# Kernel tuning notes

Hardware: AMD Instinct MI355X
Metric: run time of the kernel (lower is better)

Reference implementation:

```python
import jax, jax.numpy as jnp
import numpy as np

B = 256        # number of trees
L0 = 4096      # leaves per tree
L1 = 256       # layer-1 nodes per tree
D = 128        # input_dim == hidden_dim
OUT = 32       # output classes
EPS = 1e-5
N0 = B * L0    # 1,048,576 total leaves
N1 = B * L1    # 65,536 layer-1 nodes
N2 = B         # one root per tree


def _bn(x, g, b):
    # training-mode BatchNorm1d: biased variance over the node axis
    m = jnp.mean(x, axis=0)
    v = jnp.mean((x - m) ** 2, axis=0)
    return g * (x - m) * jax.lax.rsqrt(v + EPS) + b


def _mlp(h, w1, b1, g, beta, w2, b2):
    # GIN-style 2-layer MLP: relu(bn(linear)) -> linear
    return jax.nn.relu(_bn(h @ w1 + b1, g, beta)) @ w2 + b2


def setup_inputs() -> dict:
    key = jax.random.key(0)
    ks = jax.random.split(key, 16)

    def lin(k, fin, fout):
        kw, kb = jax.random.split(k)
        s = 1.0 / np.sqrt(fin)
        return (jax.random.uniform(kw, (fin, fout), jnp.float32, -s, s),
                jax.random.uniform(kb, (fout,), jnp.float32, -s, s))

    x = jax.random.normal(ks[0], (N0, D), jnp.float32)
    # structured tree indices: contiguous children per parent, contiguous trees
    parent1 = jnp.arange(N0, dtype=jnp.int64) // (L0 // L1)   # leaf -> layer1 parent (global)
    parent2 = jnp.arange(N1, dtype=jnp.int64) // L1           # layer1 -> root (global)
    tree0 = jnp.arange(N0, dtype=jnp.int64) // L0             # leaf -> tree id
    tree1 = jnp.arange(N1, dtype=jnp.int64) // L1             # layer1 node -> tree id

    m1w1, m1b1 = lin(ks[1], D, D)
    m1w2, m1b2 = lin(ks[2], D, D)
    m2w1, m2b1 = lin(ks[3], D, D)
    m2w2, m2b2 = lin(ks[4], D, D)
    wp, bp = lin(ks[5], D + 2 * D, OUT)

    ones = jnp.ones((D,), jnp.float32)
    zeros = jnp.zeros((D,), jnp.float32)
    return {
        "x": x, "parent1": parent1, "parent2": parent2, "tree0": tree0, "tree1": tree1,
        "mlp1_w1": m1w1, "mlp1_b1": m1b1, "mlp1_g": ones, "mlp1_beta": zeros,
        "mlp1_w2": m1w2, "mlp1_b2": m1b2, "bn1_g": ones, "bn1_b": zeros,
        "mlp2_w1": m2w1, "mlp2_b1": m2b1, "mlp2_g": ones, "mlp2_beta": zeros,
        "mlp2_w2": m2w2, "mlp2_b2": m2b2, "bn2_g": ones, "bn2_b": zeros,
        "wp": wp, "bp": bp,
    }


def reference(x, parent1, parent2, tree0, tree1,
              mlp1_w1, mlp1_b1, mlp1_g, mlp1_beta, mlp1_w2, mlp1_b2, bn1_g, bn1_b,
              mlp2_w1, mlp2_b1, mlp2_g, mlp2_beta, mlp2_w2, mlp2_b2, bn2_g, bn2_b,
              wp, bp):
    # layer 1: sparse child-sum (spmm with all-ones tree adjacency == segment_sum)
    p1 = jax.ops.segment_sum(x, parent1, num_segments=N1)              # [N1, D]
    h1 = jax.nn.relu(_bn(_mlp(p1, mlp1_w1, mlp1_b1, mlp1_g, mlp1_beta, mlp1_w2, mlp1_b2), bn1_g, bn1_b))
    # layer 2 (roots)
    p2 = jax.ops.segment_sum(h1, parent2, num_segments=N2)             # [B, D]
    h2 = jax.nn.relu(_bn(_mlp(p2, mlp2_w1, mlp2_b1, mlp2_g, mlp2_beta, mlp2_w2, mlp2_b2), bn2_g, bn2_b))
    # tree sum-pooling of layers 0..depth-1; layer depth is already per-tree
    g0 = jax.ops.segment_sum(x, tree0, num_segments=B)                 # [B, D]
    g1 = jax.ops.segment_sum(h1, tree1, num_segments=B)                # [B, D]
    rep = jnp.concatenate([g0, g1, h2], axis=1)                        # [B, 3D]
    return jax.nn.softmax(rep @ wp + bp, axis=1)                       # [B, OUT]
```

## Files before the change

kernel.cpp:

```cpp
#include <hip/hip_runtime.h>
#include <math.h>

#define D      128
#define D4     32
#define NTREE  256
#define NL1    65536
#define EPSBN  1e-5f

#define SC_OFF 0L
#define SD_OFF 256L
#define G0_OFF 512L
#define P2_OFF 33280L
#define ZERO_CNT 66048
#define SA_OFF 66048L
#define SB_OFF 66304L
#define T2_OFF 66560L
#define PBA_OFF 99328L
#define PBB_OFF 361472L
#define WT1_OFF 623616L
#define WT2_OFF 631808L
#define T1_OFF  640000L
#define U_OFF   4834304L

#define FMA4(A_, S_, W_) { (A_).x = fmaf((S_),(W_).x,(A_).x); (A_).y = fmaf((S_),(W_).y,(A_).y); \
                           (A_).z = fmaf((S_),(W_).z,(A_).z); (A_).w = fmaf((S_),(W_).w,(A_).w); }
#define ADD4(A_, B_)     { (A_).x += (B_).x; (A_).y += (B_).y; (A_).z += (B_).z; (A_).w += (B_).w; }
#define F4Z              make_float4(0.f,0.f,0.f,0.f)

typedef short  bf16x8 __attribute__((ext_vector_type(8)));
typedef float  f32x4  __attribute__((ext_vector_type(4)));

__device__ __forceinline__ unsigned short f2b(float f) {
    unsigned u = __float_as_uint(f);
    return (unsigned short)((u + 0x7FFFu + ((u >> 16) & 1u)) >> 16);
}
__device__ __forceinline__ float b2f(unsigned short h) {
    return __uint_as_float(((unsigned)h) << 16);
}

__global__ __launch_bounds__(256) void k_zp(float* __restrict__ ws,
        const float* __restrict__ w1, const float* __restrict__ w2,
        unsigned short* __restrict__ wT1, unsigned short* __restrict__ wT2)
{
    const int b = blockIdx.x, t = threadIdx.x;
    if (b < 258) {
        int i = b * 256 + t;
        if (i < ZERO_CNT) ws[i] = 0.f;
    } else {
        int idx = (b - 258) * 256 + t;
        int mat = idx >> 14;
        int e   = idx & 16383;
        int n = e >> 7, k = e & 127;
        const float* wsrc = mat ? w2 : w1;
        unsigned short* wd = mat ? wT2 : wT1;
        wd[n*128 + k] = f2b(wsrc[k*128 + n]);
    }
}

__global__ __launch_bounds__(256, 6) void k_fused1(const float* __restrict__ x,
        const unsigned short* __restrict__ wT1, const float* __restrict__ b1,
        unsigned short* __restrict__ t1, float* __restrict__ g0,
        float* __restrict__ pbufA)
{
    __shared__ __align__(16) unsigned short tileu[64][136];
    __shared__ __align__(16) float g0red[4][D];
    const int t = threadIdx.x, b = blockIdx.x;
    const int w  = t >> 6;
    const int ln = t & 63;
    const int lc = ln & 31;
    const float4* __restrict__ x4 = (const float4*)x;

    float4 gacc = F4Z;
    #pragma unroll
    for (int pp = 0; pp < 4; ++pp) {
        const int p0 = pp * 16 + w * 4;
        #pragma unroll
        for (int r = 0; r < 4; ++r) {
            const long prow = (long)b * 64 + p0 + r;
            const long base = prow * 512 + ln;
            float4 a = F4Z;
            #pragma unroll
            for (int j = 0; j < 8; ++j) { float4 v = x4[base + j * 64]; ADD4(a, v) }
            float4 o;
            o.x = __shfl_xor(a.x, 32); o.y = __shfl_xor(a.y, 32);
            o.z = __shfl_xor(a.z, 32); o.w = __shfl_xor(a.w, 32);
            ADD4(a, o)
            if (ln < 32) {
                ushort4 h;
                h.x = f2b(a.x); h.y = f2b(a.y); h.z = f2b(a.z); h.w = f2b(a.w);
                *(ushort4*)&tileu[p0 + r][lc*4] = h;
                ADD4(gacc, a)
            }
        }
    }
    if (ln < 32) *(float4*)&g0red[w][lc*4] = gacc;
    __syncthreads();
    if (t < 32) {
        float4 G = F4Z;
        #pragma unroll
        for (int g = 0; g < 4; ++g) { float4 vg = *(const float4*)&g0red[g][t*4]; ADD4(G, vg) }
        const int tree = b >> 2;
        atomicAdd(&g0[tree*D + t*4+0], G.x); atomicAdd(&g0[tree*D + t*4+1], G.y);
        atomicAdd(&g0[tree*D + t*4+2], G.z); atomicAdd(&g0[tree*D + t*4+3], G.w);
    }

    const int lq = ln >> 4;
    const int lr = ln & 15;
    bf16x8 av[4];
    #pragma unroll
    for (int ks = 0; ks < 4; ++ks)
        av[ks] = *(const bf16x8*)&tileu[w*16 + lr][ks*32 + lq*8];
    __syncthreads();

    const long rowbase = (long)b * 64;
    float sP[8], qP[8];
    #pragma unroll
    for (int cb = 0; cb < 8; ++cb) {
        f32x4 acc = {0.f, 0.f, 0.f, 0.f};
        #pragma unroll
        for (int ks = 0; ks < 4; ++ks) {
            bf16x8 bv = *(const bf16x8*)&wT1[(cb*16 + lr)*128 + ks*32 + lq*8];
            acc = __builtin_amdgcn_mfma_f32_16x16x32_bf16(av[ks], bv, acc, 0, 0, 0);
        }
        const float bc = b1[cb*16 + lr];
        float s = 0.f, q = 0.f;
        #pragma unroll
        for (int j = 0; j < 4; ++j) {
            float v = acc[j] + bc;
            t1[(rowbase + w*16 + lq*4 + j)*128 + cb*16 + lr] = f2b(v);
            s += v; q = fmaf(v, v, q);
        }
        sP[cb] = s; qP[cb] = q;
    }

    float* sq = (float*)tileu;
    #pragma unroll
    for (int cb = 0; cb < 8; ++cb) {
        sq[(w*4 + lq)*128 + cb*16 + lr]        = sP[cb];
        sq[2048 + (w*4 + lq)*128 + cb*16 + lr] = qP[cb];
    }
    __syncthreads();
    if (t < 128) {
        float S = 0.f, Q = 0.f;
        #pragma unroll
        for (int r = 0; r < 16; ++r) { S += sq[r*128 + t]; Q += sq[2048 + r*128 + t]; }
        pbufA[b*256 + t]       = S;
        pbufA[b*256 + 128 + t] = Q;
    }
}

__global__ __launch_bounds__(256) void k_statR(const float* __restrict__ pbuf,
                                               float* __restrict__ stats)
{
    __shared__ float red[8][32];
    const int t = threadIdx.x, b = blockIdx.x;
    const int c = b * 32 + (t & 31);
    const int g = t >> 5;
    float s = 0.f;
    #pragma unroll 8
    for (int r = g; r < 1024; r += 8) s += pbuf[r*256 + c];
    red[g][t & 31] = s;
    __syncthreads();
    if (t < 32) {
        float S = 0.f;
        #pragma unroll
        for (int gg = 0; gg < 8; ++gg) S += red[gg][t];
        stats[b*32 + t] = S;
    }
}

__global__ __launch_bounds__(256, 6) void k_mm2(const unsigned short* __restrict__ t1,
        const unsigned short* __restrict__ wT2, const float* __restrict__ b2,
        const float* __restrict__ mg, const float* __restrict__ mbe,
        const float* __restrict__ statsA, unsigned short* __restrict__ u,
        float* __restrict__ pbufB)
{
    __shared__ __align__(16) unsigned short tileu[64][136];
    const int t = threadIdx.x, b = blockIdx.x;
    const int tc = t & 31, rg = t >> 5;
    const long base = (long)b * 64;

    float4 scv, shv;
    {
        const float inv = 1.f / (float)NL1;
        #pragma unroll
        for (int i = 0; i < 4; ++i) {
            const int c = tc*4 + i;
            float m  = statsA[c] * inv;
            float vv = statsA[D + c] * inv - m * m;
            float rs = rsqrtf(vv + EPSBN);
            float sc = mg[c] * rs;
            ((float*)&scv)[i] = sc;
            ((float*)&shv)[i] = mbe[c] - m * sc;
        }
    }
    #pragma unroll
    for (int i = 0; i < 8; ++i) {
        const int row = i * 8 + rg;
        ushort4 hv = *(const ushort4*)&t1[(base + row)*128 + tc*4];
        float4 y;
        y.x = fmaxf(fmaf(b2f(hv.x), scv.x, shv.x), 0.f);
        y.y = fmaxf(fmaf(b2f(hv.y), scv.y, shv.y), 0.f);
        y.z = fmaxf(fmaf(b2f(hv.z), scv.z, shv.z), 0.f);
        y.w = fmaxf(fmaf(b2f(hv.w), scv.w, shv.w), 0.f);
        ushort4 h;
        h.x = f2b(y.x); h.y = f2b(y.y); h.z = f2b(y.z); h.w = f2b(y.w);
        *(ushort4*)&tileu[row][tc*4] = h;
    }
    __syncthreads();

    const int w  = t >> 6;
    const int ln = t & 63;
    const int lq = ln >> 4, lr = ln & 15;
    bf16x8 av[4];
    #pragma unroll
    for (int ks = 0; ks < 4; ++ks)
        av[ks] = *(const bf16x8*)&tileu[w*16 + lr][ks*32 + lq*8];
    __syncthreads();

    float sP[8], qP[8];
    #pragma unroll
    for (int cb = 0; cb < 8; ++cb) {
        f32x4 acc = {0.f, 0.f, 0.f, 0.f};
        #pragma unroll
        for (int ks = 0; ks < 4; ++ks) {
            bf16x8 bv = *(const bf16x8*)&wT2[(cb*16 + lr)*128 + ks*32 + lq*8];
            acc = __builtin_amdgcn_mfma_f32_16x16x32_bf16(av[ks], bv, acc, 0, 0, 0);
        }
        const float bc = b2[cb*16 + lr];
        float s = 0.f, q = 0.f;
        #pragma unroll
        for (int j = 0; j < 4; ++j) {
            float v = acc[j] + bc;
            u[(base + w*16 + lq*4 + j)*128 + cb*16 + lr] = f2b(v);
            s += v; q = fmaf(v, v, q);
        }
        sP[cb] = s; qP[cb] = q;
    }

    float* sq = (float*)tileu;
    #pragma unroll
    for (int cb = 0; cb < 8; ++cb) {
        sq[(w*4 + lq)*128 + cb*16 + lr]        = sP[cb];
        sq[2048 + (w*4 + lq)*128 + cb*16 + lr] = qP[cb];
    }
    __syncthreads();
    if (t < 128) {
        float S = 0.f, Q = 0.f;
        #pragma unroll
        for (int r = 0; r < 16; ++r) { S += sq[r*128 + t]; Q += sq[2048 + r*128 + t]; }
        pbufB[b*256 + t]       = S;
        pbufB[b*256 + 128 + t] = Q;
    }
}

__global__ __launch_bounds__(256) void k_pool(const unsigned short* __restrict__ u,
        const float* __restrict__ bg, const float* __restrict__ bb_,
        const float* __restrict__ statsB, float* __restrict__ p2)
{
    __shared__ __align__(16) float red[8][D];
    const int t = threadIdx.x, b = blockIdx.x;
    const int tree = b >> 3, chunk = b & 7;
    const int tc = t & 31, rr = t >> 5;
    const ushort4* __restrict__ uv = (const ushort4*)u;

    float4 scv, shv;
    {
        const float inv = 1.f / (float)NL1;
        #pragma unroll
        for (int i = 0; i < 4; ++i) {
            const int c = tc*4 + i;
            float m  = statsB[c] * inv;
            float vv = statsB[D + c] * inv - m * m;
            float rs = rsqrtf(vv + EPSBN);
            float sc = bg[c] * rs;
            ((float*)&scv)[i] = sc;
            ((float*)&shv)[i] = bb_[c] - m * sc;
        }
    }
    const long rbase = (long)tree * 256 + chunk * 32;
    float4 ps = F4Z;
    #pragma unroll
    for (int i = 0; i < 4; ++i) {
        const int row = i * 8 + rr;
        ushort4 hv = uv[(rbase + row) * D4 + tc];
        float4 v = make_float4(b2f(hv.x), b2f(hv.y), b2f(hv.z), b2f(hv.w));
        ps.x += fmaxf(fmaf(v.x, scv.x, shv.x), 0.f);
        ps.y += fmaxf(fmaf(v.y, scv.y, shv.y), 0.f);
        ps.z += fmaxf(fmaf(v.z, scv.z, shv.z), 0.f);
        ps.w += fmaxf(fmaf(v.w, scv.w, shv.w), 0.f);
    }
    *(float4*)&red[rr][tc*4] = ps;
    __syncthreads();
    if (t < 32) {
        float4 S = F4Z;
        #pragma unroll
        for (int g = 0; g < 8; ++g) { float4 vs = *(const float4*)&red[g][t*4]; ADD4(S, vs) }
        atomicAdd(&p2[tree*D + t*4+0], S.x); atomicAdd(&p2[tree*D + t*4+1], S.y);
        atomicAdd(&p2[tree*D + t*4+2], S.z); atomicAdd(&p2[tree*D + t*4+3], S.w);
    }
}

__global__ __launch_bounds__(256) void k_root1(const float* __restrict__ p2,
        const float* __restrict__ w1, const float* __restrict__ b1,
        float* __restrict__ t2, float* __restrict__ statsC)
{
    __shared__ __align__(16) float ps[8][D];
    __shared__ __align__(16) float red[2][8][D];
    const int t = threadIdx.x, b = blockIdx.x;
    const int j4 = t & 31, rr = t >> 5;
    *(float4*)&ps[rr][j4*4] = ((const float4*)p2)[(b*8 + rr)*D4 + j4];
    __syncthreads();
    const int row = t >> 5, tc = t & 31;
    const float4* wv = (const float4*)w1;
    float4 acc = ((const float4*)b1)[tc];
    #pragma unroll 8
    for (int k4 = 0; k4 < 32; ++k4) {
        float4 a = *(const float4*)&ps[row][k4*4];
        float4 wr0 = wv[(k4*4+0)*D4 + tc];
        float4 wr1 = wv[(k4*4+1)*D4 + tc];
        float4 wr2 = wv[(k4*4+2)*D4 + tc];
        float4 wr3 = wv[(k4*4+3)*D4 + tc];
        FMA4(acc, a.x, wr0) FMA4(acc, a.y, wr1) FMA4(acc, a.z, wr2) FMA4(acc, a.w, wr3)
    }
    ((float4*)t2)[(b*8 + row)*D4 + tc] = acc;
    float4 q;
    q.x = acc.x*acc.x; q.y = acc.y*acc.y; q.z = acc.z*acc.z; q.w = acc.w*acc.w;
    *(float4*)&red[0][row][tc*4] = acc;
    *(float4*)&red[1][row][tc*4] = q;
    __syncthreads();
    if (t < D) {
        float S = 0.f, Q = 0.f;
        #pragma unroll
        for (int g = 0; g < 8; ++g) { S += red[0][g][t]; Q += red[1][g][t]; }
        atomicAdd(&statsC[t], S);
        atomicAdd(&statsC[D+t], Q);
    }
}

__global__ __launch_bounds__(256) void k_root2(float* __restrict__ t2,
        const float* __restrict__ mg, const float* __restrict__ mb,
        const float* __restrict__ statsC,
        const float* __restrict__ w2, const float* __restrict__ b2,
        float* __restrict__ statsD)
{
    __shared__ __align__(16) float ysr[8][D];
    __shared__ __align__(16) float red[2][8][D];
    __shared__ __align__(16) float scs[D], shs[D];
    const int t = threadIdx.x, b = blockIdx.x;
    if (t < D) {
        float m = statsC[t] * (1.f / 256.f);
        float v = statsC[D+t] * (1.f / 256.f) - m * m;
        float rs = rsqrtf(v + EPSBN);
        float sc = mg[t] * rs;
        scs[t] = sc;
        shs[t] = mb[t] - m * sc;
    }
    __syncthreads();
    const int j4 = t & 31, rr = t >> 5;
    {
        float4 uu = ((const float4*)t2)[(b*8 + rr)*D4 + j4];
        float4 sc4 = *(const float4*)&scs[j4*4];
        float4 sh4 = *(const float4*)&shs[j4*4];
        float4 y;
        y.x = fmaxf(fmaf(uu.x, sc4.x, sh4.x), 0.f);
        y.y = fmaxf(fmaf(uu.y, sc4.y, sh4.y), 0.f);
        y.z = fmaxf(fmaf(uu.z, sc4.z, sh4.z), 0.f);
        y.w = fmaxf(fmaf(uu.w, sc4.w, sh4.w), 0.f);
        *(float4*)&ysr[rr][j4*4] = y;
    }
    __syncthreads();
    const int row = t >> 5, tc = t & 31;
    const float4* wv = (const float4*)w2;
    float4 acc = ((const float4*)b2)[tc];
    #pragma unroll 8
    for (int k4 = 0; k4 < 32; ++k4) {
        float4 a = *(const float4*)&ysr[row][k4*4];
        float4 wr0 = wv[(k4*4+0)*D4 + tc];
        float4 wr1 = wv[(k4*4+1)*D4 + tc];
        float4 wr2 = wv[(k4*4+2)*D4 + tc];
        float4 wr3 = wv[(k4*4+3)*D4 + tc];
        FMA4(acc, a.x, wr0) FMA4(acc, a.y, wr1) FMA4(acc, a.z, wr2) FMA4(acc, a.w, wr3)
    }
    ((float4*)t2)[(b*8 + row)*D4 + tc] = acc;
    float4 q;
    q.x = acc.x*acc.x; q.y = acc.y*acc.y; q.z = acc.z*acc.z; q.w = acc.w*acc.w;
    *(float4*)&red[0][row][tc*4] = acc;
    *(float4*)&red[1][row][tc*4] = q;
    __syncthreads();
    if (t < D) {
        float S = 0.f, Q = 0.f;
        #pragma unroll
        for (int g = 0; g < 8; ++g) { S += red[0][g][t]; Q += red[1][g][t]; }
        atomicAdd(&statsD[t], S);
        atomicAdd(&statsD[D+t], Q);
    }
}

__global__ __launch_bounds__(128) void k_final(const float* __restrict__ u2,
        const float* __restrict__ statsD,
        const float* __restrict__ bg, const float* __restrict__ bb_,
        const float* __restrict__ g0, const float* __restrict__ p2,
        const float* __restrict__ wp, const float* __restrict__ bp,
        float* __restrict__ out)
{
    __shared__ __align__(16) float reps[3*D];
    const int t = threadIdx.x, tree = blockIdx.x;
    if (t < D) {
        float m = statsD[t] * (1.f / 256.f);
        float v = statsD[D+t] * (1.f / 256.f) - m * m;
        float rs = rsqrtf(v + EPSBN);
        float sc = bg[t] * rs;
        float sh = bb_[t] - m * sc;
        reps[2*D + t] = fmaxf(fmaf(u2[tree*D + t], sc, sh), 0.f);
        reps[t]       = g0[tree*D + t];
        reps[D + t]   = p2[tree*D + t];
    }
    __syncthreads();
    if (t < 32) {
        float acc = bp[t];
        #pragma unroll 8
        for (int j = 0; j < 3*D; ++j) acc = fmaf(reps[j], wp[j*32 + t], acc);
        float mx = acc;
        #pragma unroll
        for (int mk = 16; mk > 0; mk >>= 1) mx = fmaxf(mx, __shfl_xor(mx, mk));
        float e = expf(acc - mx);
        float s = e;
        #pragma unroll
        for (int mk = 16; mk > 0; mk >>= 1) s += __shfl_xor(s, mk);
        out[tree*32 + t] = e / s;
    }
}

extern "C" void kernel_launch(void* const* d_in, const int* in_sizes, int n_in,
                              void* d_out, int out_size, void* d_ws, size_t ws_size,
                              hipStream_t stream)
{
    const float* x    = (const float*)d_in[0];
    const float* m1w1 = (const float*)d_in[5];
    const float* m1b1 = (const float*)d_in[6];
    const float* m1g  = (const float*)d_in[7];
    const float* m1be = (const float*)d_in[8];
    const float* m1w2 = (const float*)d_in[9];
    const float* m1b2 = (const float*)d_in[10];
    const float* bn1g = (const float*)d_in[11];
    const float* bn1b = (const float*)d_in[12];
    const float* m2w1 = (const float*)d_in[13];
    const float* m2b1 = (const float*)d_in[14];
    const float* m2g  = (const float*)d_in[15];
    const float* m2be = (const float*)d_in[16];
    const float* m2w2 = (const float*)d_in[17];
    const float* m2b2 = (const float*)d_in[18];
    const float* bn2g = (const float*)d_in[19];
    const float* bn2b = (const float*)d_in[20];
    const float* wp   = (const float*)d_in[21];
    const float* bp   = (const float*)d_in[22];
    float* out = (float*)d_out;
    float* ws  = (float*)d_ws;

    float* sC  = ws + SC_OFF;
    float* sD  = ws + SD_OFF;
    float* g0  = ws + G0_OFF;
    float* p2  = ws + P2_OFF;
    float* sA  = ws + SA_OFF;
    float* sB  = ws + SB_OFF;
    float* t2  = ws + T2_OFF;
    float* pbA = ws + PBA_OFF;
    float* pbB = ws + PBB_OFF;
    unsigned short* wT1 = (unsigned short*)(ws + WT1_OFF);
    unsigned short* wT2 = (unsigned short*)(ws + WT2_OFF);
    unsigned short* t1  = (unsigned short*)(ws + T1_OFF);
    unsigned short* u   = (unsigned short*)(ws + U_OFF);

    hipLaunchKernelGGL(k_zp,     dim3(386),  dim3(256), 0, stream, ws, m1w1, m1w2, wT1, wT2);
    hipLaunchKernelGGL(k_fused1, dim3(1024), dim3(256), 0, stream, x, wT1, m1b1, t1, g0, pbA);
    hipLaunchKernelGGL(k_statR,  dim3(8),    dim3(256), 0, stream, pbA, sA);
    hipLaunchKernelGGL(k_mm2,    dim3(1024), dim3(256), 0, stream, t1, wT2, m1b2, m1g, m1be, sA, u, pbB);
    hipLaunchKernelGGL(k_statR,  dim3(8),    dim3(256), 0, stream, pbB, sB);
    hipLaunchKernelGGL(k_pool,   dim3(2048), dim3(256), 0, stream, u, bn1g, bn1b, sB, p2);
    hipLaunchKernelGGL(k_root1,  dim3(32),   dim3(256), 0, stream, p2, m2w1, m2b1, t2, sC);
    hipLaunchKernelGGL(k_root2,  dim3(32),   dim3(256), 0, stream, t2, m2g, m2be, sC, m2w2, m2b2, sD);
    hipLaunchKernelGGL(k_final,  dim3(256),  dim3(128), 0, stream, t2, sD, bn2g, bn2b, g0, p2, wp, bp, out);
}
```

Measured before the change: 210.9 us.

## Fold stat reductions into producers and merge root kernels via cooperative launch

The separate column-reduction kernels for the BN statistics are removed. Each producer kernel now bumps an atomic counter, and the last block to finish sums the per-block partials into the stats. The three small root/final kernels are merged into one cooperative kernel that uses grid-wide syncs, with a fallback to separate launches if the cooperative launch fails. This is meant to cut launch overhead and dependency gaps between tiny kernels. The cost is that the last-block reduction runs serially in one block, and the grid barriers add their own cost.

```diff
diff --git a/kernel.cpp b/kernel.cpp
--- a/kernel.cpp
+++ b/kernel.cpp
@@ -1,5 +1,8 @@
 #include <hip/hip_runtime.h>
+#include <hip/hip_cooperative_groups.h>
 #include <math.h>
+
+namespace cg = cooperative_groups;
 
 #define D      128
 #define D4     32
@@ -7,20 +10,21 @@
 #define NL1    65536
 #define EPSBN  1e-5f
 
-#define SC_OFF 0L
-#define SD_OFF 256L
-#define G0_OFF 512L
-#define P2_OFF 33280L
-#define ZERO_CNT 66048
-#define SA_OFF 66048L
-#define SB_OFF 66304L
-#define T2_OFF 66560L
-#define PBA_OFF 99328L
-#define PBB_OFF 361472L
-#define WT1_OFF 623616L
-#define WT2_OFF 631808L
-#define T1_OFF  640000L
-#define U_OFF   4834304L
+#define SC_OFF  0L
+#define SD_OFF  256L
+#define G0_OFF  512L
+#define P2_OFF  33280L
+#define CNT_OFF 66048L
+#define ZERO_CNT 66056
+#define SA_OFF  66304L
+#define SB_OFF  66560L
+#define T2_OFF  66816L
+#define PBA_OFF 99584L
+#define PBB_OFF 361728L
+#define WT1_OFF 623872L
+#define WT2_OFF 632064L
+#define T1_OFF  640256L
+#define U_OFF   4834560L
 
 #define FMA4(A_, S_, W_) { (A_).x = fmaf((S_),(W_).x,(A_).x); (A_).y = fmaf((S_),(W_).y,(A_).y); \
                            (A_).z = fmaf((S_),(W_).z,(A_).z); (A_).w = fmaf((S_),(W_).w,(A_).w); }
@@ -43,11 +47,11 @@
         unsigned short* __restrict__ wT1, unsigned short* __restrict__ wT2)
 {
     const int b = blockIdx.x, t = threadIdx.x;
-    if (b < 258) {
+    if (b < 259) {
         int i = b * 256 + t;
         if (i < ZERO_CNT) ws[i] = 0.f;
     } else {
-        int idx = (b - 258) * 256 + t;
+        int idx = (b - 259) * 256 + t;
         int mat = idx >> 14;
         int e   = idx & 16383;
         int n = e >> 7, k = e & 127;
@@ -60,10 +64,12 @@
 __global__ __launch_bounds__(256, 6) void k_fused1(const float* __restrict__ x,
         const unsigned short* __restrict__ wT1, const float* __restrict__ b1,
         unsigned short* __restrict__ t1, float* __restrict__ g0,
-        float* __restrict__ pbufA)
+        float* __restrict__ pbufA, int* __restrict__ cnt,
+        float* __restrict__ statsA)
 {
     __shared__ __align__(16) unsigned short tileu[64][136];
     __shared__ __align__(16) float g0red[4][D];
+    __shared__ bool amLast;
     const int t = threadIdx.x, b = blockIdx.x;
     const int w  = t >> 6;
     const int ln = t & 63;
@@ -104,8 +110,7 @@
         atomicAdd(&g0[tree*D + t*4+2], G.z); atomicAdd(&g0[tree*D + t*4+3], G.w);
     }
 
-    const int lq = ln >> 4;
-    const int lr = ln & 15;
+    const int lq = ln >> 4, lr = ln & 15;
     bf16x8 av[4];
     #pragma unroll
     for (int ks = 0; ks < 4; ++ks)
@@ -147,25 +152,16 @@
         pbufA[b*256 + t]       = S;
         pbufA[b*256 + 128 + t] = Q;
     }
-}
-
-__global__ __launch_bounds__(256) void k_statR(const float* __restrict__ pbuf,
-                                               float* __restrict__ stats)
-{
-    __shared__ float red[8][32];
-    const int t = threadIdx.x, b = blockIdx.x;
-    const int c = b * 32 + (t & 31);
-    const int g = t >> 5;
-    float s = 0.f;
-    #pragma unroll 8
-    for (int r = g; r < 1024; r += 8) s += pbuf[r*256 + c];
-    red[g][t & 31] = s;
-    __syncthreads();
-    if (t < 32) {
+
+    __threadfence();
+    if (t == 0) amLast = (atomicAdd(cnt, 1) == 1023);
+    __syncthreads();
+    if (amLast) {
+        __threadfence();
         float S = 0.f;
-        #pragma unroll
-        for (int gg = 0; gg < 8; ++gg) S += red[gg][t];
-        stats[b*32 + t] = S;
+        #pragma unroll 8
+        for (int r = 0; r < 1024; ++r) S += pbufA[r*256 + t];
+        statsA[t] = S;
     }
 }
 
@@ -173,9 +169,11 @@
         const unsigned short* __restrict__ wT2, const float* __restrict__ b2,
         const float* __restrict__ mg, const float* __restrict__ mbe,
         const float* __restrict__ statsA, unsigned short* __restrict__ u,
-        float* __restrict__ pbufB)
+        float* __restrict__ pbufB, int* __restrict__ cnt,
+        float* __restrict__ statsB)
 {
     __shared__ __align__(16) unsigned short tileu[64][136];
+    __shared__ bool amLast;
     const int t = threadIdx.x, b = blockIdx.x;
     const int tc = t & 31, rg = t >> 5;
     const long base = (long)b * 64;
@@ -252,6 +250,17 @@
         pbufB[b*256 + t]       = S;
         pbufB[b*256 + 128 + t] = Q;
     }
+
+    __threadfence();
+    if (t == 0) amLast = (atomicAdd(cnt, 1) == 1023);
+    __syncthreads();
+    if (amLast) {
+        __threadfence();
+        float S = 0.f;
+        #pragma unroll 8
+        for (int r = 0; r < 1024; ++r) S += pbufB[r*256 + t];
+        statsB[t] = S;
+    }
 }
 
 __global__ __launch_bounds__(256) void k_pool(const unsigned short* __restrict__ u,
@@ -301,13 +310,11 @@
     }
 }
 
-__global__ __launch_bounds__(256) void k_root1(const float* __restrict__ p2,
+__device__ __forceinline__ void root1_body(const float* __restrict__ p2,
         const float* __restrict__ w1, const float* __restrict__ b1,
-        float* __restrict__ t2, float* __restrict__ statsC)
-{
-    __shared__ __align__(16) float ps[8][D];
-    __shared__ __align__(16) float red[2][8][D];
-    const int t = threadIdx.x, b = blockIdx.x;
+        float* __restrict__ t2, float* __restrict__ statsC,
+        float (*ps)[D], float (*red)[8][D], int t, int b)
+{
     const int j4 = t & 31, rr = t >> 5;
     *(float4*)&ps[rr][j4*4] = ((const float4*)p2)[(b*8 + rr)*D4 + j4];
     __syncthreads();
@@ -338,16 +345,13 @@
     }
 }
 
-__global__ __launch_bounds__(256) void k_root2(float* __restrict__ t2,
+__device__ __forceinline__ void root2_body(float* __restrict__ t2,
         const float* __restrict__ mg, const float* __restrict__ mb,
         const float* __restrict__ statsC,
         const float* __restrict__ w2, const float* __restrict__ b2,
-        float* __restrict__ statsD)
-{
-    __shared__ __align__(16) float ysr[8][D];
-    __shared__ __align__(16) float red[2][8][D];
-    __shared__ __align__(16) float scs[D], shs[D];
-    const int t = threadIdx.x, b = blockIdx.x;
+        float* __restrict__ statsD,
+        float (*ysr)[D], float (*red)[8][D], float* scs, float* shs, int t, int b)
+{
     if (t < D) {
         float m = statsC[t] * (1.f / 256.f);
         float v = statsC[D+t] * (1.f / 256.f) - m * m;
@@ -397,15 +401,13 @@
     }
 }
 
-__global__ __launch_bounds__(128) void k_final(const float* __restrict__ u2,
+__device__ __forceinline__ void final_body(const float* __restrict__ u2,
         const float* __restrict__ statsD,
         const float* __restrict__ bg, const float* __restrict__ bb_,
         const float* __restrict__ g0, const float* __restrict__ p2,
         const float* __restrict__ wp, const float* __restrict__ bp,
-        float* __restrict__ out)
-{
-    __shared__ __align__(16) float reps[3*D];
-    const int t = threadIdx.x, tree = blockIdx.x;
+        float* __restrict__ out, float* reps, int t, int tree)
+{
     if (t < D) {
         float m = statsD[t] * (1.f / 256.f);
         float v = statsD[D+t] * (1.f / 256.f) - m * m;
@@ -430,6 +432,64 @@
         for (int mk = 16; mk > 0; mk >>= 1) s += __shfl_xor(s, mk);
         out[tree*32 + t] = e / s;
     }
+}
+
+__global__ __launch_bounds__(256) void k_rootfin(const float* __restrict__ p2,
+        const float* __restrict__ w1, const float* __restrict__ b1,
+        const float* __restrict__ mg, const float* __restrict__ mbe,
+        const float* __restrict__ w2, const float* __restrict__ b2,
+        const float* __restrict__ bg, const float* __restrict__ bb_,
+        const float* __restrict__ g0, const float* __restrict__ wp,
+        const float* __restrict__ bp,
+        float* __restrict__ t2, float* __restrict__ statsC,
+        float* __restrict__ statsD, float* __restrict__ out)
+{
+    cg::grid_group grid = cg::this_grid();
+    __shared__ __align__(16) float ps[8][D];
+    __shared__ __align__(16) float red[2][8][D];
+    __shared__ __align__(16) float scs[D], shs[D];
+    __shared__ __align__(16) float reps[3*D];
+    const int t = threadIdx.x, b = blockIdx.x;
+
+    if (b < 32) root1_body(p2, w1, b1, t2, statsC, ps, red, t, b);
+    grid.sync();
+    if (b < 32) root2_body(t2, mg, mbe, statsC, w2, b2, statsD, ps, red, scs, shs, t, b);
+    grid.sync();
+    final_body(t2, statsD, bg, bb_, g0, p2, wp, bp, out, reps, t, b);
+}
+
+__global__ __launch_bounds__(256) void k_root1(const float* __restrict__ p2,
+        const float* __restrict__ w1, const float* __restrict__ b1,
+        float* __restrict__ t2, float* __restrict__ statsC)
+{
+    __shared__ __align__(16) float ps[8][D];
+    __shared__ __align__(16) float red[2][8][D];
+    root1_body(p2, w1, b1, t2, statsC, ps, red, threadIdx.x, blockIdx.x);
+}
+
+__global__ __launch_bounds__(256) void k_root2(float* __restrict__ t2,
+        const float* __restrict__ mg, const float* __restrict__ mb,
+        const float* __restrict__ statsC,
+        const float* __restrict__ w2, const float* __restrict__ b2,
+        float* __restrict__ statsD)
+{
+    __shared__ __align__(16) float ysr[8][D];
+    __shared__ __align__(16) float red[2][8][D];
+    __shared__ __align__(16) float scs[D], shs[D];
+    root2_body(t2, mg, mb, statsC, w2, b2, statsD, ysr, red, scs, shs,
+               threadIdx.x, blockIdx.x);
+}
+
+__global__ __launch_bounds__(128) void k_final(const float* __restrict__ u2,
+        const float* __restrict__ statsD,
+        const float* __restrict__ bg, const float* __restrict__ bb_,
+        const float* __restrict__ g0, const float* __restrict__ p2,
+        const float* __restrict__ wp, const float* __restrict__ bp,
+        float* __restrict__ out)
+{
+    __shared__ __align__(16) float reps[3*D];
+    final_body(u2, statsD, bg, bb_, g0, p2, wp, bp, out, reps,
+               threadIdx.x, blockIdx.x);
 }
 
 extern "C" void kernel_launch(void* const* d_in, const int* in_sizes, int n_in,
@@ -462,6 +522,7 @@
     float* sD  = ws + SD_OFF;
     float* g0  = ws + G0_OFF;
     float* p2  = ws + P2_OFF;
+    int*   cnt = (int*)(ws + CNT_OFF);
     float* sA  = ws + SA_OFF;
     float* sB  = ws + SB_OFF;
     float* t2  = ws + T2_OFF;
@@ -472,13 +533,22 @@
     unsigned short* t1  = (unsigned short*)(ws + T1_OFF);
     unsigned short* u   = (unsigned short*)(ws + U_OFF);
 
-    hipLaunchKernelGGL(k_zp,     dim3(386),  dim3(256), 0, stream, ws, m1w1, m1w2, wT1, wT2);
-    hipLaunchKernelGGL(k_fused1, dim3(1024), dim3(256), 0, stream, x, wT1, m1b1, t1, g0, pbA);
-    hipLaunchKernelGGL(k_statR,  dim3(8),    dim3(256), 0, stream, pbA, sA);
-    hipLaunchKernelGGL(k_mm2,    dim3(1024), dim3(256), 0, stream, t1, wT2, m1b2, m1g, m1be, sA, u, pbB);
-    hipLaunchKernelGGL(k_statR,  dim3(8),    dim3(256), 0, stream, pbB, sB);
+    hipLaunchKernelGGL(k_zp,     dim3(387),  dim3(256), 0, stream, ws, m1w1, m1w2, wT1, wT2);
+    hipLaunchKernelGGL(k_fused1, dim3(1024), dim3(256), 0, stream,
+                       x, wT1, m1b1, t1, g0, pbA, cnt, sA);
+    hipLaunchKernelGGL(k_mm2,    dim3(1024), dim3(256), 0, stream,
+                       t1, wT2, m1b2, m1g, m1be, sA, u, pbB, cnt + 1, sB);
     hipLaunchKernelGGL(k_pool,   dim3(2048), dim3(256), 0, stream, u, bn1g, bn1b, sB, p2);
-    hipLaunchKernelGGL(k_root1,  dim3(32),   dim3(256), 0, stream, p2, m2w1, m2b1, t2, sC);
-    hipLaunchKernelGGL(k_root2,  dim3(32),   dim3(256), 0, stream, t2, m2g, m2be, sC, m2w2, m2b2, sD);
-    hipLaunchKernelGGL(k_final,  dim3(256),  dim3(128), 0, stream, t2, sD, bn2g, bn2b, g0, p2, wp, bp, out);
-}
+
+    void* args[] = { (void*)&p2, (void*)&m2w1, (void*)&m2b1, (void*)&m2g, (void*)&m2be,
+                     (void*)&m2w2, (void*)&m2b2, (void*)&bn2g, (void*)&bn2b,
+                     (void*)&g0, (void*)&wp, (void*)&bp,
+                     (void*)&t2, (void*)&sC, (void*)&sD, (void*)&out };
+    hipError_t ce = hipLaunchCooperativeKernel((void*)k_rootfin, dim3(256), dim3(256),
+                                               args, 0, stream);
+    if (ce != hipSuccess) {
+        hipLaunchKernelGGL(k_root1, dim3(32),  dim3(256), 0, stream, p2, m2w1, m2b1, t2, sC);
+        hipLaunchKernelGGL(k_root2, dim3(32),  dim3(256), 0, stream, t2, m2g, m2be, sC, m2w2, m2b2, sD);
+        hipLaunchKernelGGL(k_final, dim3(256), dim3(128), 0, stream, t2, sD, bn2g, bn2b, g0, p2, wp, bp, out);
+    }
+}
```

After: 569.8 us. 170% more time.
